# Kernel optimization log

Measured on AMD Instinct MI355X. Metric: run time of the kernel, lower is better.

## Reference

```python
import jax, jax.numpy as jnp
import numpy as np
from jax import lax

B, C, H, W = 8, 256, 64, 64
O, K, E = 256, 3, 3  # out_channels, kernel_size, num_experts

def setup_inputs() -> dict:
    key = jax.random.key(0)
    k1, k2, k3, k4, k5 = jax.random.split(key, 5)
    q = jax.random.normal(k1, (B, C, H, W), dtype=jnp.float32)
    y = jax.random.normal(k2, (B, C, H, W), dtype=jnp.float32)
    experts = jax.random.normal(k3, (E, O, 2 * C, K, K), dtype=jnp.float32)
    # torch nn.Linear(2C, E): store transposed [2C, E] for ctx @ gate_w
    bound = 1.0 / np.sqrt(2 * C)
    gate_w = jax.random.uniform(k4, (2 * C, E), minval=-bound, maxval=bound, dtype=jnp.float32)
    gate_b = jax.random.uniform(k5, (E,), minval=-bound, maxval=bound, dtype=jnp.float32)
    return {"q": q, "y": y, "experts": experts, "gate_w": gate_w, "gate_b": gate_b}

def reference(q, y, experts, gate_w, gate_b):
    # gate: softmax over experts from global-avg-pooled context of y (duplicated)
    y_ctx = jnp.mean(y, axis=(2, 3))                       # [B, C]
    context = jnp.concatenate([y_ctx, y_ctx], axis=1)       # [B, 2C]
    gates = jax.nn.softmax(context @ gate_w + gate_b, axis=1)  # [B, E]
    # per-sample fused kernel: sum_e gates[b,e] * experts[e]  -> [B, O, 2C, K, K]
    w = jnp.einsum('be,eoikl->boikl', gates, experts)
    xy = jnp.concatenate([q, q], axis=1)                     # [B, 2C, H, W]
    # batched dynamic conv via grouped conv: batch -> groups (no Python loop)
    b, c2, h, wd = xy.shape
    x1 = xy.reshape(1, b * c2, h, wd)
    w1 = w.reshape(b * O, c2, K, K)
    out = lax.conv_general_dilated(
        x1, w1, window_strides=(1, 1), padding='SAME',
        dimension_numbers=('NCHW', 'OIHW', 'NCHW'),
        feature_group_count=b)
    return out.reshape(b, O, h, wd)
```

## Files before the change

kernel.cpp:

```cpp
#include <hip/hip_runtime.h>
#include <hip/hip_bf16.h>
#include <math.h>


typedef __bf16 bf16x8 __attribute__((ext_vector_type(8)));
typedef __bf16 bf16x4 __attribute__((ext_vector_type(4)));
typedef float f32x4 __attribute__((ext_vector_type(4)));

#define AS1 __attribute__((address_space(1)))
#define AS3 __attribute__((address_space(3)))

__global__ __launch_bounds__(64) void yctx_kernel(const float* __restrict__ y,
                                                  float* __restrict__ yctx) {
  int bc = blockIdx.x;
  const float4* p = (const float4*)(y + (size_t)bc * 4096);
  int lane = threadIdx.x;
  float s = 0.f;
  for (int i = lane; i < 1024; i += 64) {
    float4 v = p[i];
    s += v.x + v.y + v.z + v.w;
  }
#pragma unroll
  for (int off = 32; off > 0; off >>= 1) s += __shfl_down(s, off, 64);
  if (lane == 0) yctx[bc] = s * (1.f / 4096.f);
}

__global__ __launch_bounds__(64) void logits_kernel(const float* __restrict__ yctx,
                                                    const float* __restrict__ gw,
                                                    const float* __restrict__ gb,
                                                    float* __restrict__ logits) {
  int be = blockIdx.x;
  int b = be / 3, e = be - b * 3;
  int lane = threadIdx.x;
  float s = 0.f;
  for (int c = lane; c < 256; c += 64)
    s += yctx[b * 256 + c] * (gw[c * 3 + e] + gw[(c + 256) * 3 + e]);
#pragma unroll
  for (int off = 32; off > 0; off >>= 1) s += __shfl_down(s, off, 64);
  if (lane == 0) logits[be] = s + gb[e];
}

__global__ __launch_bounds__(256) void wbuild_kernel(const float* __restrict__ experts,
                                                     const float* __restrict__ logits,
                                                     __bf16* __restrict__ wf) {
  int o = blockIdx.x;
  int tid = threadIdx.x;
  __shared__ float sf[3][2304];
  __shared__ float g[8][3];

#pragma unroll
  for (int e = 0; e < 3; e++) {
    const float4* src = (const float4*)(experts + ((size_t)e * 256 + o) * 4608);
    float4* dstp = (float4*)sf[e];
    for (int i = tid; i < 576; i += 256) {
      float4 a = src[i], bq = src[i + 576];
      float4 r;
      r.x = a.x + bq.x; r.y = a.y + bq.y; r.z = a.z + bq.z; r.w = a.w + bq.w;
      dstp[i] = r;
    }
  }
  if (tid < 8) {
    float l0 = logits[tid * 3 + 0], l1 = logits[tid * 3 + 1], l2 = logits[tid * 3 + 2];
    float m = fmaxf(l0, fmaxf(l1, l2));
    float e0 = __expf(l0 - m), e1 = __expf(l1 - m), e2 = __expf(l2 - m);
    float inv = 1.f / (e0 + e1 + e2);
    g[tid][0] = e0 * inv; g[tid][1] = e1 * inv; g[tid][2] = e2 * inv;
  }
  __syncthreads();

  int cl = tid & 31, ch = tid >> 5;
#pragma unroll 1
  for (int b = 0; b < 8; b++) {
    float g0 = g[b][0], g1 = g[b][1], g2 = g[b][2];
#pragma unroll
    for (int tap = 0; tap < 9; tap++) {
      float v = g0 * sf[0][tid * 9 + tap] + g1 * sf[1][tid * 9 + tap] +
                g2 * sf[2][tid * 9 + tap];
      wf[((((size_t)b * 9 + tap) * 8 + ch) * 256 + o) * 32 + cl] = (__bf16)v;
    }
  }
}

__global__ __launch_bounds__(256) void qt_kernel(const float* __restrict__ q,
                                                 __bf16* __restrict__ qT) {
  int bid = blockIdx.x;
  int hp = bid % 66;
  int t2 = bid / 66;
  int ch = t2 & 7;
  int b = t2 >> 3;
  __bf16* dst = qT + (((size_t)(b * 8 + ch) * 66 + hp) * 66) * 32;
  int tid = threadIdx.x;
  float4 z4 = {0.f, 0.f, 0.f, 0.f};
  if (hp == 0 || hp == 65) {
    float4* d4 = (float4*)dst;
    for (int i = tid; i < 264; i += 256) d4[i] = z4;
    return;
  }
  __shared__ float tile2[64][33];
  int h = hp - 1;
  {
    int w = tid & 63, ci = tid >> 6;
#pragma unroll
    for (int j = 0; j < 8; j++) {
      int c = ci * 8 + j;
      tile2[w][c] = q[(((size_t)b * 256 + ch * 32 + c) * 64 + h) * 64 + w];
    }
  }
  if (tid < 4) ((float4*)dst)[tid] = z4;
  else if (tid < 8) ((float4*)(dst + 65 * 32))[tid - 4] = z4;
  __syncthreads();

  int a = tid & 7, wsl = tid >> 3;
  int cl4 = a * 4;
#pragma unroll
  for (int k = 0; k < 2; k++) {
    int w = wsl * 2 + k, wp = w + 1;
    int clp4 = (((cl4 >> 3) ^ ((wp >> 1) & 3)) << 3) | (cl4 & 7);
    float v0 = tile2[w][cl4 + 0], v1 = tile2[w][cl4 + 1];
    float v2 = tile2[w][cl4 + 2], v3 = tile2[w][cl4 + 3];
    bf16x4 r = {(__bf16)v0, (__bf16)v1, (__bf16)v2, (__bf16)v3};
    *(bf16x4*)(dst + wp * 32 + clp4) = r;
  }
}

__global__ __launch_bounds__(256) void conv_kernel(const __bf16* __restrict__ qT,
                                                   const __bf16* __restrict__ wf,
                                                   float* __restrict__ out) {
  __shared__ __align__(16) __bf16 Qlds[2][4 * 66 * 32];
  const int tid = threadIdx.x;
  const int lane = tid & 63;
  const int wv = tid >> 6;
  const int wm = wv >> 1, wn = wv & 1;
  const int l15 = lane & 15, qd = lane >> 4;

  const int bid = blockIdx.x;
  const int b = bid & 7;
  const int rem = bid >> 3;
  const int o0 = (rem >> 5) * 128;
  const int h0 = (rem & 31) * 2;

  f32x4 acc[4][4];
  {
    f32x4 z = {0.f, 0.f, 0.f, 0.f};
#pragma unroll
    for (int i = 0; i < 4; i++)
#pragma unroll
      for (int j = 0; j < 4; j++) acc[i][j] = z;
  }

  const char* qT_b = (const char*)qT + (size_t)b * 8 * 66 * 66 * 32 * 2;
  const char* abase = (const char*)wf + ((size_t)b * 9 * 8 * 256 +
                                         (size_t)(o0 + wm * 64 + l15)) * 64 +
                      (size_t)qd * 16;
  bf16x8 acur[4], anxt[4];

  {
    const char* qsrc = qT_b + ((size_t)h0) * 66 * 32 * 2;
    for (int i = tid; i < 1056; i += 256) {
      int ub = i - lane;
      __builtin_amdgcn_global_load_lds((const AS1 void*)(qsrc + ((size_t)i << 4)),
                                       (AS3 void*)((char*)Qlds[0] + ((size_t)ub << 4)),
                                       16, 0, 0);
    }
#pragma unroll
    for (int mi = 0; mi < 4; mi++)
      acur[mi] = *(const bf16x8*)(abase + mi * 1024);
    __syncthreads();
  }

#pragma unroll 1
  for (int ch = 0; ch < 8; ch++) {
    if (ch < 7) {
      const char* qsrc = qT_b + ((size_t)(ch + 1) * 66 + h0) * 66 * 32 * 2;
      char* qdst = (char*)Qlds[(ch + 1) & 1];
      for (int i = tid; i < 1056; i += 256) {
        int ub = i - lane;
        __builtin_amdgcn_global_load_lds((const AS1 void*)(qsrc + ((size_t)i << 4)),
                                         (AS3 void*)(qdst + ((size_t)ub << 4)),
                                         16, 0, 0);
      }
    }
    const char* Qb = (const char*)Qlds[ch & 1];
#pragma unroll
    for (int tap = 0; tap < 9; tap++) {
      {
        int tapn = (tap == 8) ? 0 : tap + 1;
        int chn = (tap == 8) ? ch + 1 : ch;
        size_t aoff = ((size_t)(tapn * 8 + chn)) << 14;
#pragma unroll
        for (int mi = 0; mi < 4; mi++)
          anxt[mi] = *(const bf16x8*)(abase + aoff + mi * 1024);
      }
      const int dh = tap / 3, dw = tap - dh * 3;
      const int r = wn + dh;
#pragma unroll
      for (int ni = 0; ni < 4; ni++) {
        int wp = ni * 16 + l15 + dw;
        int g = (qd ^ ((wp >> 1) & 3)) << 3;
        bf16x8 bfv = *(const bf16x8*)(Qb + ((r * 66 + wp) * 32 + g) * 2);
#pragma unroll
        for (int mi = 0; mi < 4; mi++)
          acc[mi][ni] = __builtin_amdgcn_mfma_f32_16x16x32_bf16(
              acur[mi], bfv, acc[mi][ni], 0, 0, 0);
      }
#pragma unroll
      for (int mi = 0; mi < 4; mi++) acur[mi] = anxt[mi];
    }
    __syncthreads();
  }

  const int hh = h0 + wn;
#pragma unroll
  for (int mi = 0; mi < 4; mi++) {
    int o = o0 + wm * 64 + mi * 16 + qd * 4;
#pragma unroll
    for (int ni = 0; ni < 4; ni++) {
      int w = ni * 16 + l15;
#pragma unroll
      for (int rr = 0; rr < 4; rr++)
        out[(((size_t)b * 256 + (o + rr)) * 64 + hh) * 64 + w] = acc[mi][ni][rr];
    }
  }
}

extern "C" void kernel_launch(void* const* d_in, const int* in_sizes, int n_in,
                              void* d_out, int out_size, void* d_ws, size_t ws_size,
                              hipStream_t stream) {
  (void)in_sizes; (void)n_in; (void)out_size; (void)ws_size;
  const float* q = (const float*)d_in[0];
  const float* y = (const float*)d_in[1];
  const float* experts = (const float*)d_in[2];
  const float* gate_w = (const float*)d_in[3];
  const float* gate_b = (const float*)d_in[4];
  float* out = (float*)d_out;

  char* ws = (char*)d_ws;
  float* yctx = (float*)ws;
  float* logits = (float*)(ws + 8192);
  __bf16* wf = (__bf16*)(ws + 16384);
  __bf16* qT = (__bf16*)(ws + 16384 + 9437184);

  yctx_kernel<<<2048, 64, 0, stream>>>(y, yctx);
  logits_kernel<<<24, 64, 0, stream>>>(yctx, gate_w, gate_b, logits);
  qt_kernel<<<8 * 8 * 66, 256, 0, stream>>>(q, qT);
  wbuild_kernel<<<256, 256, 0, stream>>>(experts, logits, wf);
  conv_kernel<<<512, 256, 0, stream>>>(qT, wf, out);
}
```

Measured before the change: 178.3 us.

## Deepen conv register pipelining: prefetch weights two taps ahead and LDS one tap

The conv kernel now triple-buffers the global weight fragments, so they load two taps ahead instead of one. It also double-buffers the LDS input fragments, loading the next tap's B operands before the current tap's MFMAs and the first tap of the next channel right after the barrier. LDS byte offsets per dw/ni are precomputed once into a small table, and launch bounds request two blocks per CU. The aim is to hide global and LDS latency behind the MFMAs, at the cost of more registers. If the runtime-dependent modulo buffer index is not folded, there is a risk of register spills or scratch use.

```diff
diff --git a/kernel.cpp b/kernel.cpp
--- a/kernel.cpp
+++ b/kernel.cpp
@@ -123,9 +123,9 @@
   }
 }
 
-__global__ __launch_bounds__(256) void conv_kernel(const __bf16* __restrict__ qT,
-                                                   const __bf16* __restrict__ wf,
-                                                   float* __restrict__ out) {
+__global__ __launch_bounds__(256, 2) void conv_kernel(const __bf16* __restrict__ qT,
+                                                      const __bf16* __restrict__ wf,
+                                                      float* __restrict__ out) {
   __shared__ __align__(16) __bf16 Qlds[2][4 * 66 * 32];
   const int tid = threadIdx.x;
   const int lane = tid & 63;
@@ -148,14 +148,25 @@
       for (int j = 0; j < 4; j++) acc[i][j] = z;
   }
 
+  int btab[3][4];
+#pragma unroll
+  for (int dw = 0; dw < 3; dw++)
+#pragma unroll
+    for (int ni = 0; ni < 4; ni++) {
+      int wp = ni * 16 + l15 + dw;
+      int g = (qd ^ ((wp >> 1) & 3)) << 3;
+      btab[dw][ni] = (wp * 32 + g) * 2;
+    }
+
   const char* qT_b = (const char*)qT + (size_t)b * 8 * 66 * 66 * 32 * 2;
   const char* abase = (const char*)wf + ((size_t)b * 9 * 8 * 256 +
                                          (size_t)(o0 + wm * 64 + l15)) * 64 +
                       (size_t)qd * 16;
-  bf16x8 acur[4], anxt[4];
+  bf16x8 areg[3][4];
+  bf16x8 breg[2][4];
 
   {
-    const char* qsrc = qT_b + ((size_t)h0) * 66 * 32 * 2;
+    const char* qsrc = qT_b + ((size_t)h0) * 4224;
     for (int i = tid; i < 1056; i += 256) {
       int ub = i - lane;
       __builtin_amdgcn_global_load_lds((const AS1 void*)(qsrc + ((size_t)i << 4)),
@@ -163,15 +174,20 @@
                                        16, 0, 0);
     }
 #pragma unroll
-    for (int mi = 0; mi < 4; mi++)
-      acur[mi] = *(const bf16x8*)(abase + mi * 1024);
+    for (int mi = 0; mi < 4; mi++) {
+      areg[0][mi] = *(const bf16x8*)(abase + ((size_t)(0 * 8 + 0) << 14) + mi * 1024);
+      areg[1][mi] = *(const bf16x8*)(abase + ((size_t)(1 * 8 + 0) << 14) + mi * 1024);
+    }
     __syncthreads();
+#pragma unroll
+    for (int ni = 0; ni < 4; ni++)
+      breg[0][ni] = *(const bf16x8*)((const char*)Qlds[0] + wn * 4224 + btab[0][ni]);
   }
 
 #pragma unroll 1
   for (int ch = 0; ch < 8; ch++) {
     if (ch < 7) {
-      const char* qsrc = qT_b + ((size_t)(ch + 1) * 66 + h0) * 66 * 32 * 2;
+      const char* qsrc = qT_b + ((size_t)((ch + 1) * 66 + h0)) * 4224;
       char* qdst = (char*)Qlds[(ch + 1) & 1];
       for (int i = tid; i < 1056; i += 256) {
         int ub = i - lane;
@@ -183,30 +199,38 @@
     const char* Qb = (const char*)Qlds[ch & 1];
 #pragma unroll
     for (int tap = 0; tap < 9; tap++) {
+      const int s = ch * 9 + tap;
       {
-        int tapn = (tap == 8) ? 0 : tap + 1;
-        int chn = (tap == 8) ? ch + 1 : ch;
-        size_t aoff = ((size_t)(tapn * 8 + chn)) << 14;
+        int s2 = s + 2;
+        int ch2 = s2 / 9, tap2 = s2 - ch2 * 9;
+        if (ch2 > 7) { ch2 = 0; tap2 = 0; }
+        size_t aoff = ((size_t)(tap2 * 8 + ch2)) << 14;
 #pragma unroll
         for (int mi = 0; mi < 4; mi++)
-          anxt[mi] = *(const bf16x8*)(abase + aoff + mi * 1024);
+          areg[(s + 2) % 3][mi] = *(const bf16x8*)(abase + aoff + mi * 1024);
       }
-      const int dh = tap / 3, dw = tap - dh * 3;
-      const int r = wn + dh;
-#pragma unroll
-      for (int ni = 0; ni < 4; ni++) {
-        int wp = ni * 16 + l15 + dw;
-        int g = (qd ^ ((wp >> 1) & 3)) << 3;
-        bf16x8 bfv = *(const bf16x8*)(Qb + ((r * 66 + wp) * 32 + g) * 2);
+      if (tap < 8) {
+        int tapn = tap + 1;
+        int dhn = tapn / 3, dwn = tapn - dhn * 3;
+        int rbn = (wn + dhn) * 4224;
+#pragma unroll
+        for (int ni = 0; ni < 4; ni++)
+          breg[(tap + 1) & 1][ni] = *(const bf16x8*)(Qb + rbn + btab[dwn][ni]);
+      }
+#pragma unroll
+      for (int ni = 0; ni < 4; ni++)
 #pragma unroll
         for (int mi = 0; mi < 4; mi++)
           acc[mi][ni] = __builtin_amdgcn_mfma_f32_16x16x32_bf16(
-              acur[mi], bfv, acc[mi][ni], 0, 0, 0);
-      }
-#pragma unroll
-      for (int mi = 0; mi < 4; mi++) acur[mi] = anxt[mi];
+              areg[s % 3][mi], breg[tap & 1][ni], acc[mi][ni], 0, 0, 0);
     }
     __syncthreads();
+    if (ch < 7) {
+      const char* Qn = (const char*)Qlds[(ch + 1) & 1];
+#pragma unroll
+      for (int ni = 0; ni < 4; ni++)
+        breg[0][ni] = *(const bf16x8*)(Qn + wn * 4224 + btab[0][ni]);
+    }
   }
 
   const int hh = h0 + wn;
```

Result: slower. 182.9 us (+2.6%).
